# Kernel tuning notes

Hardware: AMD Instinct MI355X
Metric: run time of the kernel (lower is better)

The kernel has to match this reference:

```python
import jax, jax.numpy as jnp
import numpy as np

ALPHA = 2.0   # spikingjelly surrogate.ATan default
TAU = 2.0     # LIFNode default
VTH = 1.0     # v_threshold
T = 16

@jax.custom_vjp
def atan_spike(u):
    # heaviside forward, ATan surrogate backward
    return (u >= 0).astype(u.dtype)

def _atan_fwd(u):
    return atan_spike(u), u

def _atan_bwd(u, g):
    return (g * (ALPHA / 2.0) / (1.0 + (jnp.pi / 2.0 * ALPHA * u) ** 2),)

atan_spike.defvjp(_atan_fwd, _atan_bwd)


def setup_inputs() -> dict:
    key = jax.random.key(0)
    ks = jax.random.split(key, 7)
    n_in, n_hid, n_out, B = 512, 1024, 6, 16384

    def lin(k, fan_in, shape):
        bound = 1.0 / np.sqrt(fan_in)
        return jax.random.uniform(k, shape, jnp.float32, -bound, bound)

    return {
        "x": jax.random.normal(ks[0], (B, n_in), jnp.float32),
        "W1": lin(ks[1], n_in, (n_hid, n_in)),
        "b1": lin(ks[2], n_in, (n_hid,)),
        "W2": lin(ks[3], n_hid, (n_hid, n_hid)),
        "b2": lin(ks[4], n_hid, (n_hid,)),
        "W3": lin(ks[5], n_hid, (n_out, n_hid)),
        "b3": lin(ks[6], n_hid, (n_out,)),
    }


def reference(x, W1, b1, W2, b2, W3, b3):
    # Input is static across timesteps -> fc1 output is loop-invariant.
    i1 = x @ W1.T + b1  # [B, n_hid]
    B = x.shape[0]
    init = (
        jnp.zeros((B, W1.shape[0]), x.dtype),  # v1
        jnp.zeros((B, W2.shape[0]), x.dtype),  # v2
        jnp.zeros((B, W3.shape[0]), x.dtype),  # v3
    )

    def lif(v, i):
        # charge: v += (i - (v - v_reset)) / tau, v_reset = 0
        v = v + (i - v) / TAU
        s = atan_spike(v - VTH)
        # hard reset to v_reset = 0 (detach_reset=False -> keep grad path)
        v = v * (1.0 - s)
        return v, s

    def step(carry, _):
        v1, v2, v3 = carry
        v1, s1 = lif(v1, i1)
        v2, s2 = lif(v2, s1 @ W2.T + b2)
        v3, s3 = lif(v3, s2 @ W3.T + b3)
        return (v1, v2, v3), s3

    _, spikes = jax.lax.scan(step, init, None, length=T)  # [T, B, n_out]
    return spikes.sum(axis=0) / T
```

## Files before the change

kernel.cpp:

```cpp
#include <hip/hip_runtime.h>
#include <hip/hip_bf16.h>


typedef _Float16 f16;
typedef __attribute__((ext_vector_type(4))) _Float16 f16x4;
typedef __attribute__((ext_vector_type(8))) _Float16 f16x8;
typedef __attribute__((ext_vector_type(4))) float f32x4;

__global__ __launch_bounds__(256) void k_cvt(const float* __restrict__ x,
                                             const float* __restrict__ W1,
                                             f16* __restrict__ xh,
                                             f16* __restrict__ W1h) {
    const int NX = 16384 * 512 / 4;
    const int NW = 1024 * 512 / 4;
    int i = blockIdx.x * 256 + threadIdx.x;
    const int stride = gridDim.x * 256;
    for (; i < NX + NW; i += stride) {
        const float4* src;
        f16* dst;
        int j;
        if (i < NX) { src = (const float4*)x; dst = xh; j = i; }
        else        { src = (const float4*)W1; dst = W1h; j = i - NX; }
        float4 v = src[j];
        f16x4 h;
        h.x = (f16)v.x; h.y = (f16)v.y; h.z = (f16)v.z; h.w = (f16)v.w;
        *(f16x4*)(dst + (size_t)4 * j) = h;
    }
}

__global__ void k_tq(const float* __restrict__ W2, unsigned char* __restrict__ W2u) {
    __shared__ float t[32][33];
    const int bj = blockIdx.x;
    const int bk = blockIdx.y;
    const int tx = threadIdx.x;
    const int ty = threadIdx.y;
#pragma unroll
    for (int i = 0; i < 32; i += 8)
        t[ty + i][tx] = W2[(size_t)(bj * 32 + ty + i) * 1024 + bk * 32 + tx];
    __syncthreads();
#pragma unroll
    for (int i = 0; i < 32; i += 8) {
        float v = t[tx][ty + i];
        int q = (int)rintf(v * 4064.0f);
        q = q > 127 ? 127 : (q < -127 ? -127 : q);
        W2u[(size_t)(bk * 32 + ty + i) * 1024 + bj * 32 + tx] = (unsigned char)(q + 128);
    }
}

__global__ __launch_bounds__(256) void k_fc1(const f16* __restrict__ xh,
                                             const f16* __restrict__ W1h,
                                             const float* __restrict__ b1,
                                             f16* __restrict__ i1h) {
    __shared__ __align__(16) f16 Atile[128 * 32];
    __shared__ __align__(16) f16 Btile[256 * 32];
    const int tid = threadIdx.x;
    const int lane = tid & 63;
    const int wid = tid >> 6;
    const int wm = wid >> 1;
    const int wn = wid & 1;
    const int m0 = blockIdx.x * 128;
    const int n0 = blockIdx.y * 256;

    f32x4 acc[4][8] = {};

    for (int k0 = 0; k0 < 512; k0 += 32) {
        __syncthreads();
#pragma unroll
        for (int q = 0; q < 6; ++q) {
            const bool isA = (q < 2);
            int u = q * 256 + tid;
            int cu = isA ? u : (u - 512);
            int rl = cu >> 2;
            int slot = (cu & 3) ^ (rl & 3);
            const f16* g = isA
                ? xh  + (size_t)(m0 + rl) * 512 + k0 + slot * 8
                : W1h + (size_t)(n0 + rl) * 512 + k0 + slot * 8;
            f16x8 v = *(const f16x8*)g;
            f16* d = (isA ? Atile : Btile) + (size_t)cu * 8;
            *(f16x8*)d = v;
        }
        __syncthreads();
        f16x8 af[4], bf[8];
#pragma unroll
        for (int i = 0; i < 4; ++i) {
            int rowA = (wm << 6) + (i << 4) + (lane & 15);
            af[i] = *(const f16x8*)(Atile + rowA * 32 + (((lane >> 4) ^ (rowA & 3)) << 3));
        }
#pragma unroll
        for (int j = 0; j < 8; ++j) {
            int rowB = (wn << 7) + (j << 4) + (lane & 15);
            bf[j] = *(const f16x8*)(Btile + rowB * 32 + (((lane >> 4) ^ (rowB & 3)) << 3));
        }
#pragma unroll
        for (int i = 0; i < 4; ++i)
#pragma unroll
            for (int j = 0; j < 8; ++j)
                acc[i][j] = __builtin_amdgcn_mfma_f32_16x16x32_f16(af[i], bf[j], acc[i][j], 0, 0, 0);
    }

    float b1v[8];
#pragma unroll
    for (int j = 0; j < 8; ++j)
        b1v[j] = b1[n0 + (wn << 7) + (j << 4) + (lane & 15)];
#pragma unroll
    for (int i = 0; i < 4; ++i) {
        int rm = m0 + (wm << 6) + (i << 4) + ((lane >> 4) << 2);
#pragma unroll
        for (int j = 0; j < 8; ++j) {
            int cn = n0 + (wn << 7) + (j << 4) + (lane & 15);
            f16* op = i1h + (size_t)rm * 1024 + cn;
#pragma unroll
            for (int rr = 0; rr < 4; ++rr)
                op[(size_t)rr * 1024] = (f16)(acc[i][j][rr] + b1v[j]);
        }
    }
}

__global__ __launch_bounds__(256) void k_snn(const f16* __restrict__ i1g,
                                             const unsigned char* __restrict__ W2u,
                                             const float* __restrict__ b2,
                                             const float* __restrict__ W3,
                                             const float* __restrict__ b3,
                                             float* __restrict__ out) {
    const int lane = threadIdx.x & 63;
    const int wid = threadIdx.x >> 6;
    const int r = blockIdx.x * 4 + wid;
    const float DEQ = 1.0f / 4064.0f;

    float i1r[4][4];
    const f16* i1row = i1g + (size_t)r * 1024;
#pragma unroll
    for (int g = 0; g < 4; ++g) {
        f16x4 t = *(const f16x4*)(i1row + 4 * lane + 256 * g);
        i1r[g][0] = (float)t.x; i1r[g][1] = (float)t.y;
        i1r[g][2] = (float)t.z; i1r[g][3] = (float)t.w;
    }
    float b2r[16];
#pragma unroll
    for (int q = 0; q < 4; ++q) {
        float4 u = ((const float4*)b2)[lane * 4 + q];
        b2r[4 * q + 0] = u.x; b2r[4 * q + 1] = u.y;
        b2r[4 * q + 2] = u.z; b2r[4 * q + 3] = u.w;
    }
    float b3r[6];
#pragma unroll
    for (int m6 = 0; m6 < 6; ++m6) b3r[m6] = b3[m6];

    const uint4* w2v = (const uint4*)W2u;

    float v1[4][4] = {}, v2[16] = {}, v3[6] = {}, cnt[6] = {};

    for (int t = 0; t < 16; ++t) {
        unsigned accE[4] = {0u, 0u, 0u, 0u};
        unsigned accO[4] = {0u, 0u, 0u, 0u};
        int nrows = 0;
#pragma unroll
        for (int g = 0; g < 4; ++g)
#pragma unroll
            for (int e = 0; e < 4; ++e) {
                float v = v1[g][e];
                v = v + (i1r[g][e] - v) * 0.5f;
                bool s = v >= 1.0f;
                v1[g][e] = s ? 0.0f : v;
                unsigned long long m = __ballot(s ? 1 : 0);
                nrows += (int)__popcll(m);
                while (m) {
                    int b0 = __builtin_ctzll(m);
                    m &= m - 1;
                    uint4 w0 = w2v[(size_t)(4 * b0 + 256 * g + e) * 64 + lane];
                    bool have1 = (m != 0ull);
                    uint4 w1;
                    if (have1) {
                        int b1i = __builtin_ctzll(m);
                        m &= m - 1;
                        w1 = w2v[(size_t)(4 * b1i + 256 * g + e) * 64 + lane];
                    }
                    accE[0] += __builtin_amdgcn_perm(0u, w0.x, 0x04020400u);
                    accO[0] += __builtin_amdgcn_perm(0u, w0.x, 0x04030401u);
                    accE[1] += __builtin_amdgcn_perm(0u, w0.y, 0x04020400u);
                    accO[1] += __builtin_amdgcn_perm(0u, w0.y, 0x04030401u);
                    accE[2] += __builtin_amdgcn_perm(0u, w0.z, 0x04020400u);
                    accO[2] += __builtin_amdgcn_perm(0u, w0.z, 0x04030401u);
                    accE[3] += __builtin_amdgcn_perm(0u, w0.w, 0x04020400u);
                    accO[3] += __builtin_amdgcn_perm(0u, w0.w, 0x04030401u);
                    if (have1) {
                        accE[0] += __builtin_amdgcn_perm(0u, w1.x, 0x04020400u);
                        accO[0] += __builtin_amdgcn_perm(0u, w1.x, 0x04030401u);
                        accE[1] += __builtin_amdgcn_perm(0u, w1.y, 0x04020400u);
                        accO[1] += __builtin_amdgcn_perm(0u, w1.y, 0x04030401u);
                        accE[2] += __builtin_amdgcn_perm(0u, w1.z, 0x04020400u);
                        accO[2] += __builtin_amdgcn_perm(0u, w1.z, 0x04030401u);
                        accE[3] += __builtin_amdgcn_perm(0u, w1.w, 0x04020400u);
                        accO[3] += __builtin_amdgcn_perm(0u, w1.w, 0x04030401u);
                    }
                }
            }
        const int bias = nrows << 7;
        bool s2[16];
#pragma unroll
        for (int d = 0; d < 4; ++d) {
            int sq0 = (int)(accE[d] & 0xFFFFu) - bias;
            int sq1 = (int)(accO[d] & 0xFFFFu) - bias;
            int sq2 = (int)(accE[d] >> 16) - bias;
            int sq3 = (int)(accO[d] >> 16) - bias;
            int sq[4] = {sq0, sq1, sq2, sq3};
#pragma unroll
            for (int c = 0; c < 4; ++c) {
                int e = 4 * d + c;
                float i2 = fmaf((float)sq[c], DEQ, b2r[e]);
                float v = v2[e];
                v = v + (i2 - v) * 0.5f;
                bool s = v >= 1.0f;
                s2[e] = s;
                v2[e] = s ? 0.0f : v;
            }
        }
        float i3[6];
#pragma unroll
        for (int m6 = 0; m6 < 6; ++m6) i3[m6] = b3r[m6];
#pragma unroll
        for (int e = 0; e < 16; ++e) {
            unsigned long long m = __ballot(s2[e] ? 1 : 0);
            while (m) {
                int b = __builtin_ctzll(m);
                m &= m - 1;
                int j = 16 * b + e;
#pragma unroll
                for (int m6 = 0; m6 < 6; ++m6) i3[m6] += W3[m6 * 1024 + j];
            }
        }
#pragma unroll
        for (int m6 = 0; m6 < 6; ++m6) {
            float v = v3[m6];
            v = v + (i3[m6] - v) * 0.5f;
            bool s = v >= 1.0f;
            cnt[m6] += s ? 1.0f : 0.0f;
            v3[m6] = s ? 0.0f : v;
        }
    }
    if (lane == 0) {
#pragma unroll
        for (int m6 = 0; m6 < 6; ++m6)
            out[(size_t)r * 6 + m6] = cnt[m6] * 0.0625f;
    }
}

extern "C" void kernel_launch(void* const* d_in, const int* in_sizes, int n_in,
                              void* d_out, int out_size, void* d_ws, size_t ws_size,
                              hipStream_t stream) {
    const float* x  = (const float*)d_in[0];
    const float* W1 = (const float*)d_in[1];
    const float* b1 = (const float*)d_in[2];
    const float* W2 = (const float*)d_in[3];
    const float* b2 = (const float*)d_in[4];
    const float* W3 = (const float*)d_in[5];
    const float* b3 = (const float*)d_in[6];
    float* out = (float*)d_out;

    char* ws = (char*)d_ws;
    f16* i1h = (f16*)ws;
    f16* xh  = (f16*)(ws + ((size_t)32 << 20));
    f16* W1h = (f16*)(ws + ((size_t)48 << 20));
    unsigned char* W2u = (unsigned char*)(ws + ((size_t)49 << 20));

    k_cvt<<<2048, 256, 0, stream>>>(x, W1, xh, W1h);
    k_tq<<<dim3(32, 32), dim3(32, 8), 0, stream>>>(W2, W2u);
    k_fc1<<<dim3(128, 4), 256, 0, stream>>>(xh, W1h, b1, i1h);
    k_snn<<<4096, 256, 0, stream>>>(i1h, W2u, b2, W3, b3, out);
}
```

Before: 440.2 us.

## Precompute layer-1 spike trains and reuse W2 row loads across eight timesteps

Layer-1 LIF dynamics depend only on the constant fc1 input, so each neuron's 16-step spike train is computed up front as a bitmask, and per-timestep spike counts are reduced once with shuffles. The W2 gather then runs in two halves of eight timesteps: each W2 row is loaded once per half and added into per-timestep accumulators selected by the neuron's spike bits. This cuts repeated global loads of the same W2 rows across timesteps. In exchange it uses many more registers (8x4x2 accumulators) and a per-bit branch inside the accumulation loop, which may lower occupancy.

```diff
diff --git a/kernel.cpp b/kernel.cpp
--- a/kernel.cpp
+++ b/kernel.cpp
@@ -127,14 +127,34 @@
     const int r = blockIdx.x * 4 + wid;
     const float DEQ = 1.0f / 4064.0f;
 
-    float i1r[4][4];
-    const f16* i1row = i1g + (size_t)r * 1024;
+    unsigned train[16];
+    unsigned cnt[8] = {};
+    const f16x4* i1p4 = (const f16x4*)(i1g + (size_t)r * 1024);
 #pragma unroll
     for (int g = 0; g < 4; ++g) {
-        f16x4 t = *(const f16x4*)(i1row + 4 * lane + 256 * g);
-        i1r[g][0] = (float)t.x; i1r[g][1] = (float)t.y;
-        i1r[g][2] = (float)t.z; i1r[g][3] = (float)t.w;
-    }
+        f16x4 tq = i1p4[lane + 64 * g];
+#pragma unroll
+        for (int e = 0; e < 4; ++e) {
+            float iv = (float)tq[e];
+            float v = 0.0f;
+            unsigned tr = 0u;
+#pragma unroll
+            for (int t = 0; t < 16; ++t) {
+                v = v + (iv - v) * 0.5f;
+                unsigned su = (v >= 1.0f) ? 1u : 0u;
+                v = su ? 0.0f : v;
+                tr |= su << t;
+                cnt[t >> 1] += su << ((t & 1) * 16);
+            }
+            train[4 * g + e] = tr;
+        }
+    }
+#pragma unroll
+    for (int st = 1; st < 64; st <<= 1)
+#pragma unroll
+        for (int h = 0; h < 8; ++h)
+            cnt[h] += __shfl_xor(cnt[h], st, 64);
+
     float b2r[16];
 #pragma unroll
     for (int q = 0; q < 4; ++q) {
@@ -148,100 +168,122 @@
 
     const uint4* w2v = (const uint4*)W2u;
 
-    float v1[4][4] = {}, v2[16] = {}, v3[6] = {}, cnt[6] = {};
-
-    for (int t = 0; t < 16; ++t) {
-        unsigned accE[4] = {0u, 0u, 0u, 0u};
-        unsigned accO[4] = {0u, 0u, 0u, 0u};
-        int nrows = 0;
+    float v2[16] = {}, v3[6] = {}, cnt3[6] = {};
+
+#pragma unroll
+    for (int half = 0; half < 2; ++half) {
+        unsigned accE[8][4] = {};
+        unsigned accO[8][4] = {};
 #pragma unroll
         for (int g = 0; g < 4; ++g)
 #pragma unroll
             for (int e = 0; e < 4; ++e) {
-                float v = v1[g][e];
-                v = v + (i1r[g][e] - v) * 0.5f;
-                bool s = v >= 1.0f;
-                v1[g][e] = s ? 0.0f : v;
-                unsigned long long m = __ballot(s ? 1 : 0);
-                nrows += (int)__popcll(m);
-                while (m) {
-                    int b0 = __builtin_ctzll(m);
-                    m &= m - 1;
+                unsigned sub = (train[4 * g + e] >> (half * 8)) & 0xFFu;
+                unsigned long long m = __ballot(sub != 0u);
+                if (m) {
+                    int b0 = __builtin_ctzll(m); m &= m - 1;
+                    unsigned tr0 = __builtin_amdgcn_readlane(sub, b0);
                     uint4 w0 = w2v[(size_t)(4 * b0 + 256 * g + e) * 64 + lane];
-                    bool have1 = (m != 0ull);
-                    uint4 w1;
-                    if (have1) {
-                        int b1i = __builtin_ctzll(m);
-                        m &= m - 1;
-                        w1 = w2v[(size_t)(4 * b1i + 256 * g + e) * 64 + lane];
+                    while (m) {
+                        int b1 = __builtin_ctzll(m); m &= m - 1;
+                        unsigned tr1 = __builtin_amdgcn_readlane(sub, b1);
+                        uint4 w1 = w2v[(size_t)(4 * b1 + 256 * g + e) * 64 + lane];
+                        {
+                            unsigned E[4], O[4];
+                            E[0] = __builtin_amdgcn_perm(0u, w0.x, 0x04020400u);
+                            O[0] = __builtin_amdgcn_perm(0u, w0.x, 0x04030401u);
+                            E[1] = __builtin_amdgcn_perm(0u, w0.y, 0x04020400u);
+                            O[1] = __builtin_amdgcn_perm(0u, w0.y, 0x04030401u);
+                            E[2] = __builtin_amdgcn_perm(0u, w0.z, 0x04020400u);
+                            O[2] = __builtin_amdgcn_perm(0u, w0.z, 0x04030401u);
+                            E[3] = __builtin_amdgcn_perm(0u, w0.w, 0x04020400u);
+                            O[3] = __builtin_amdgcn_perm(0u, w0.w, 0x04030401u);
+#pragma unroll
+                            for (int tt = 0; tt < 8; ++tt)
+                                if (tr0 & (1u << tt)) {
+#pragma unroll
+                                    for (int d = 0; d < 4; ++d) {
+                                        accE[tt][d] += E[d];
+                                        accO[tt][d] += O[d];
+                                    }
+                                }
+                        }
+                        tr0 = tr1; w0 = w1;
                     }
-                    accE[0] += __builtin_amdgcn_perm(0u, w0.x, 0x04020400u);
-                    accO[0] += __builtin_amdgcn_perm(0u, w0.x, 0x04030401u);
-                    accE[1] += __builtin_amdgcn_perm(0u, w0.y, 0x04020400u);
-                    accO[1] += __builtin_amdgcn_perm(0u, w0.y, 0x04030401u);
-                    accE[2] += __builtin_amdgcn_perm(0u, w0.z, 0x04020400u);
-                    accO[2] += __builtin_amdgcn_perm(0u, w0.z, 0x04030401u);
-                    accE[3] += __builtin_amdgcn_perm(0u, w0.w, 0x04020400u);
-                    accO[3] += __builtin_amdgcn_perm(0u, w0.w, 0x04030401u);
-                    if (have1) {
-                        accE[0] += __builtin_amdgcn_perm(0u, w1.x, 0x04020400u);
-                        accO[0] += __builtin_amdgcn_perm(0u, w1.x, 0x04030401u);
-                        accE[1] += __builtin_amdgcn_perm(0u, w1.y, 0x04020400u);
-                        accO[1] += __builtin_amdgcn_perm(0u, w1.y, 0x04030401u);
-                        accE[2] += __builtin_amdgcn_perm(0u, w1.z, 0x04020400u);
-                        accO[2] += __builtin_amdgcn_perm(0u, w1.z, 0x04030401u);
-                        accE[3] += __builtin_amdgcn_perm(0u, w1.w, 0x04020400u);
-                        accO[3] += __builtin_amdgcn_perm(0u, w1.w, 0x04030401u);
+                    {
+                        unsigned E[4], O[4];
+                        E[0] = __builtin_amdgcn_perm(0u, w0.x, 0x04020400u);
+                        O[0] = __builtin_amdgcn_perm(0u, w0.x, 0x04030401u);
+                        E[1] = __builtin_amdgcn_perm(0u, w0.y, 0x04020400u);
+                        O[1] = __builtin_amdgcn_perm(0u, w0.y, 0x04030401u);
+                        E[2] = __builtin_amdgcn_perm(0u, w0.z, 0x04020400u);
+                        O[2] = __builtin_amdgcn_perm(0u, w0.z, 0x04030401u);
+                        E[3] = __builtin_amdgcn_perm(0u, w0.w, 0x04020400u);
+                        O[3] = __builtin_amdgcn_perm(0u, w0.w, 0x04030401u);
+#pragma unroll
+                        for (int tt = 0; tt < 8; ++tt)
+                            if (tr0 & (1u << tt)) {
+#pragma unroll
+                                for (int d = 0; d < 4; ++d) {
+                                    accE[tt][d] += E[d];
+                                    accO[tt][d] += O[d];
+                                }
+                            }
                     }
                 }
             }
-        const int bias = nrows << 7;
-        bool s2[16];
-#pragma unroll
-        for (int d = 0; d < 4; ++d) {
-            int sq0 = (int)(accE[d] & 0xFFFFu) - bias;
-            int sq1 = (int)(accO[d] & 0xFFFFu) - bias;
-            int sq2 = (int)(accE[d] >> 16) - bias;
-            int sq3 = (int)(accO[d] >> 16) - bias;
-            int sq[4] = {sq0, sq1, sq2, sq3};
-#pragma unroll
-            for (int c = 0; c < 4; ++c) {
-                int e = 4 * d + c;
-                float i2 = fmaf((float)sq[c], DEQ, b2r[e]);
-                float v = v2[e];
-                v = v + (i2 - v) * 0.5f;
+#pragma unroll
+        for (int tt = 0; tt < 8; ++tt) {
+            const int t = half * 8 + tt;
+            const int nr = (int)((cnt[t >> 1] >> ((t & 1) * 16)) & 0xFFFFu);
+            const int bias = nr << 7;
+            bool s2[16];
+#pragma unroll
+            for (int d = 0; d < 4; ++d) {
+                int sq[4];
+                sq[0] = (int)(accE[tt][d] & 0xFFFFu) - bias;
+                sq[1] = (int)(accO[tt][d] & 0xFFFFu) - bias;
+                sq[2] = (int)(accE[tt][d] >> 16) - bias;
+                sq[3] = (int)(accO[tt][d] >> 16) - bias;
+#pragma unroll
+                for (int c = 0; c < 4; ++c) {
+                    int e = 4 * d + c;
+                    float i2 = fmaf((float)sq[c], DEQ, b2r[e]);
+                    float v = v2[e];
+                    v = v + (i2 - v) * 0.5f;
+                    bool s = v >= 1.0f;
+                    s2[e] = s;
+                    v2[e] = s ? 0.0f : v;
+                }
+            }
+            float i3[6];
+#pragma unroll
+            for (int m6 = 0; m6 < 6; ++m6) i3[m6] = b3r[m6];
+#pragma unroll
+            for (int e = 0; e < 16; ++e) {
+                unsigned long long mm = __ballot(s2[e] ? 1 : 0);
+                while (mm) {
+                    int b = __builtin_ctzll(mm);
+                    mm &= mm - 1;
+                    int j = 16 * b + e;
+#pragma unroll
+                    for (int m6 = 0; m6 < 6; ++m6) i3[m6] += W3[m6 * 1024 + j];
+                }
+            }
+#pragma unroll
+            for (int m6 = 0; m6 < 6; ++m6) {
+                float v = v3[m6];
+                v = v + (i3[m6] - v) * 0.5f;
                 bool s = v >= 1.0f;
-                s2[e] = s;
-                v2[e] = s ? 0.0f : v;
-            }
-        }
-        float i3[6];
-#pragma unroll
-        for (int m6 = 0; m6 < 6; ++m6) i3[m6] = b3r[m6];
-#pragma unroll
-        for (int e = 0; e < 16; ++e) {
-            unsigned long long m = __ballot(s2[e] ? 1 : 0);
-            while (m) {
-                int b = __builtin_ctzll(m);
-                m &= m - 1;
-                int j = 16 * b + e;
-#pragma unroll
-                for (int m6 = 0; m6 < 6; ++m6) i3[m6] += W3[m6 * 1024 + j];
-            }
-        }
-#pragma unroll
-        for (int m6 = 0; m6 < 6; ++m6) {
-            float v = v3[m6];
-            v = v + (i3[m6] - v) * 0.5f;
-            bool s = v >= 1.0f;
-            cnt[m6] += s ? 1.0f : 0.0f;
-            v3[m6] = s ? 0.0f : v;
+                cnt3[m6] += s ? 1.0f : 0.0f;
+                v3[m6] = s ? 0.0f : v;
+            }
         }
     }
     if (lane == 0) {
 #pragma unroll
         for (int m6 = 0; m6 < 6; ++m6)
-            out[(size_t)r * 6 + m6] = cnt[m6] * 0.0625f;
+            out[(size_t)r * 6 + m6] = cnt3[m6] * 0.0625f;
     }
 }
 
```

Result: faster. 380.6 us (-13.5%).
